# Performance work log

Measured on AMD Instinct MI355X. Metric: run time of the kernel, lower is better.

The kernel has to match this reference:

```python
import jax, jax.numpy as jnp
import numpy as np

NEG_SLOPE = 0.01  # jax.nn.leaky_relu default

def bicubic_resize(x, target_h, target_w):
    # NHWC bicubic resize with antialiasing (matches original module)
    b, h, w, c = x.shape
    return jax.image.resize(x, shape=(b, target_h, target_w, c), method='bicubic', antialias=True)

def setup_inputs() -> dict:
    key = jax.random.key(0)
    x = jax.random.normal(key, (16, 128, 128, 128), dtype=jnp.float32)  # NHWC
    return {"x": x, "in_size": 128, "out_size": 128}

def reference(x, in_size, out_size):
    y = bicubic_resize(x, 2 * in_size, 2 * in_size)
    # activation on the fine grid
    y = jax.nn.leaky_relu(y, negative_slope=NEG_SLOPE)
    # downsample (antialiased) back to out_size
    y = bicubic_resize(y, out_size, out_size)
    return y
```

## Files before the change

kernel.cpp:

```cpp
#include <hip/hip_runtime.h>


#define HH 128
#define WW 128
#define CC 128
#define RS 16
#define CH 16
#define PAD 132
#define NSTEP (RS + 4)

__device__ __forceinline__ double keys_cubic(double x) {
  if (x >= 2.0) return 0.0;
  if (x >= 1.0) return ((-0.5 * x + 2.5) * x - 4.0) * x + 2.0;
  return (1.5 * x - 2.5) * x * x + 1.0;
}

__global__ __launch_bounds__(256) void fused_updown_kernel(
    const float* __restrict__ x, float* __restrict__ out) {
  __shared__ __align__(16) float wUpV[256][4];
  __shared__ __align__(16) float wDnE[4][8];
  __shared__ __align__(16) float rowv[4][CH][PAD];

  const int tid = threadIdx.x;

  {
    const int k = tid;
    const double q = 0.5 * k - 0.25;
    const int st = ((k + 1) >> 1) - 2;
    double wr[4], s = 0.0;
#pragma unroll
    for (int i = 0; i < 4; ++i) {
      const int col = st + i;
      double w = (col >= 0 && col <= 127) ? keys_cubic(fabs((double)col - q)) : 0.0;
      wr[i] = w; s += w;
    }
    const double inv = 1.0 / s;
#pragma unroll
    for (int i = 0; i < 4; ++i) wUpV[k][i] = (float)(wr[i] * inv);
  }
  if (tid < 4) {
    const int e = tid;
    const int j = (e < 2) ? e : 124 + e;
    const double p = 2.0 * j + 0.5;
    const int st = 2 * j - 3;
    double wr[8], s = 0.0;
#pragma unroll
    for (int i = 0; i < 8; ++i) {
      const int col = st + i;
      double w = (col >= 0 && col <= 255) ? keys_cubic(0.5 * fabs((double)col - p)) : 0.0;
      wr[i] = w; s += w;
    }
    const double inv = 1.0 / s;
#pragma unroll
    for (int i = 0; i < 8; ++i) wDnE[e][i] = (float)(wr[i] * inv);
  }
  __syncthreads();

  const int bid = blockIdx.x;
  const int b = bid & 15;
  const int strip = (bid >> 4) & 7;
  const int chunk = bid >> 7;
  const int oy0 = strip * RS;
  const int c0 = chunk * CH;
  const int c = tid & 15;
  const int g = tid >> 4;
  const int col0 = g * 8;
  const bool gL = (g == 0), gR = (g == 15);

  const float* xbase = x + (size_t)b * (HH * WW * CC) + (size_t)col0 * CC + (c0 + c);
  float* obase = out + (size_t)b * (HH * WW * CC) + (size_t)col0 * CC + (c0 + c);
  const int m0 = oy0 - 2;

  auto load_row = [&](float (&d)[8], int row) {
    row = row < 0 ? 0 : (row > 127 ? 127 : row);
    const float* p = xbase + (size_t)row * (WW * CC);
#pragma unroll
    for (int j = 0; j < 8; ++j) d[j] = p[j * CC];
  };

  auto wdGet = [&](int oy, float cst, int tap) -> float {
    if (oy < 0 || oy > 127) return 0.f;
    if (oy < 2) return wDnE[oy][tap];
    if (oy > 125) return wDnE[oy - 124][tap];
    return cst;
  };

  auto proc = [&](int sl, const float (&vm)[8], float w0, float w1, float w2, float w3,
                  float (&B0)[8], float (&B1)[8], float (&B2)[8], float (&B3)[8]) {
    float v[16];
    if (!gL) {
      const float4 h = *(const float4*)&rowv[sl][c][col0 - 4];
      v[0] = h.x; v[1] = h.y; v[2] = h.z; v[3] = h.w;
    } else { v[0] = v[1] = v[2] = v[3] = 0.f; }
#pragma unroll
    for (int j = 0; j < 8; ++j) v[4 + j] = vm[j];
    if (!gR) {
      const float4 h = *(const float4*)&rowv[sl][c][col0 + 8];
      v[12] = h.x; v[13] = h.y; v[14] = h.z; v[15] = h.w;
    } else { v[12] = v[13] = v[14] = v[15] = 0.f; }

    float f[22];
#pragma unroll
    for (int u = 0; u < 22; ++u) {
      const int s = (u >> 1) + 1;
      float t;
      if (u & 1)
        t = fmaf(-0.0234375f, v[s], fmaf(0.2265625f, v[s + 1],
            fmaf(0.8671875f, v[s + 2], -0.0703125f * v[s + 3])));
      else
        t = fmaf(-0.0703125f, v[s], fmaf(0.8671875f, v[s + 1],
            fmaf(0.2265625f, v[s + 2], -0.0234375f * v[s + 3])));
      f[u] = fmaxf(t, 0.01f * t);
    }
    if (gL) {
#pragma unroll
      for (int u = 3; u <= 5; ++u) {
        const int s = (u >> 1) + 1;
        const float4 w = *(const float4*)wUpV[u - 3];
        const float t = fmaf(w.x, v[s], fmaf(w.y, v[s + 1],
                        fmaf(w.z, v[s + 2], w.w * v[s + 3])));
        f[u] = fmaxf(t, 0.01f * t);
      }
    }
    if (gR) {
#pragma unroll
      for (int u = 16; u <= 18; ++u) {
        const int s = (u >> 1) + 1;
        const float4 w = *(const float4*)wUpV[237 + u];
        const float t = fmaf(w.x, v[s], fmaf(w.y, v[s + 1],
                        fmaf(w.z, v[s + 2], w.w * v[s + 3])));
        f[u] = fmaxf(t, 0.01f * t);
      }
    }
    float tt[8];
#pragma unroll
    for (int jj = 0; jj < 8; ++jj) {
      tt[jj] = fmaf(-0.01171875f, f[2 * jj] + f[2 * jj + 7],
               fmaf(-0.03515625f, f[2 * jj + 1] + f[2 * jj + 6],
               fmaf(0.11328125f, f[2 * jj + 2] + f[2 * jj + 5],
                    0.43359375f * (f[2 * jj + 3] + f[2 * jj + 4]))));
    }
    if (gL) {
#pragma unroll
      for (int jj = 0; jj < 2; ++jj) {
        float s2 = 0.f;
#pragma unroll
        for (int i = 0; i < 8; ++i) s2 = fmaf(wDnE[jj][i], f[2 * jj + i], s2);
        tt[jj] = s2;
      }
    }
    if (gR) {
#pragma unroll
      for (int jj = 6; jj < 8; ++jj) {
        float s2 = 0.f;
#pragma unroll
        for (int i = 0; i < 8; ++i) s2 = fmaf(wDnE[jj - 4][i], f[2 * jj + i], s2);
        tt[jj] = s2;
      }
    }
#pragma unroll
    for (int jj = 0; jj < 8; ++jj) {
      B0[jj] = fmaf(w0, tt[jj], B0[jj]);
      B1[jj] = fmaf(w1, tt[jj], B1[jj]);
      B2[jj] = fmaf(w2, tt[jj], B2[jj]);
      B3[jj] = fmaf(w3, tt[jj], B3[jj]);
    }
  };

  float r0[8], r1[8], r2[8], r3[8], r4[8];
  float A0[8], A1[8], A2[8], A3[8], A4[8];
#pragma unroll
  for (int i = 0; i < 8; ++i) { A0[i]=0.f; A1[i]=0.f; A2[i]=0.f; A3[i]=0.f; A4[i]=0.f; }

  load_row(r0, m0 - 2);
  load_row(r1, m0 - 1);
  load_row(r2, m0);
  load_row(r3, m0 + 1);
  load_row(r4, m0 + 2);

  for (int t = 0; t < NSTEP; ++t) {
    const int m = m0 + t;
    if (t > 0) {
#pragma unroll
      for (int i = 0; i < 8; ++i) { r0[i]=r1[i]; r1[i]=r2[i]; r2[i]=r3[i]; r3[i]=r4[i]; }
      load_row(r4, m + 2);
    }
    const bool mOK = (m >= 0) && (m <= 127);
    const bool evOK = mOK && (t >= 1);
    const bool odOK = mOK && (t <= RS + 2);
    const int sp = (t & 1) * 2;
    float vE[8], vO[8];
    if (evOK) {
      const float4 wv = *(const float4*)wUpV[2 * m];
#pragma unroll
      for (int j = 0; j < 8; ++j)
        vE[j] = fmaf(wv.x, r0[j], fmaf(wv.y, r1[j], fmaf(wv.z, r2[j], wv.w * r3[j])));
      *(float4*)&rowv[sp][c][col0]     = make_float4(vE[0], vE[1], vE[2], vE[3]);
      *(float4*)&rowv[sp][c][col0 + 4] = make_float4(vE[4], vE[5], vE[6], vE[7]);
    }
    if (odOK) {
      const float4 wv = *(const float4*)wUpV[2 * m + 1];
#pragma unroll
      for (int j = 0; j < 8; ++j)
        vO[j] = fmaf(wv.x, r1[j], fmaf(wv.y, r2[j], fmaf(wv.z, r3[j], wv.w * r4[j])));
      *(float4*)&rowv[sp + 1][c][col0]     = make_float4(vO[0], vO[1], vO[2], vO[3]);
      *(float4*)&rowv[sp + 1][c][col0 + 4] = make_float4(vO[4], vO[5], vO[6], vO[7]);
    }
    __syncthreads();
    if (evOK)
      proc(sp, vE, wdGet(m - 2, -0.01171875f, 7), wdGet(m - 1, 0.11328125f, 5),
           wdGet(m, 0.43359375f, 3), wdGet(m + 1, -0.03515625f, 1),
           A0, A1, A2, A3);
    if (odOK)
      proc(sp + 1, vO, wdGet(m - 1, -0.03515625f, 6), wdGet(m, 0.43359375f, 4),
           wdGet(m + 1, 0.11328125f, 2), wdGet(m + 2, -0.01171875f, 0),
           A1, A2, A3, A4);
    if (m - 2 >= oy0) {
      float* op = obase + (size_t)(m - 2) * (WW * CC);
#pragma unroll
      for (int jj = 0; jj < 8; ++jj) op[jj * CC] = A0[jj];
    }
#pragma unroll
    for (int jj = 0; jj < 8; ++jj) { A0[jj]=A1[jj]; A1[jj]=A2[jj]; A2[jj]=A3[jj]; A3[jj]=A4[jj]; A4[jj]=0.f; }
  }
}

extern "C" void kernel_launch(void* const* d_in, const int* in_sizes, int n_in,
                              void* d_out, int out_size, void* d_ws, size_t ws_size,
                              hipStream_t stream) {
  const float* x = (const float*)d_in[0];
  float* o = (float*)d_out;
  dim3 grid(16 * 8 * 8);
  dim3 block(256);
  hipLaunchKernelGGL(fused_updown_kernel, grid, block, 0, stream, x, o);
}
```

Measured before the change: 105.1 us.

## Pack even/odd fine rows as float2 to use packed FP32 math

Computes the even and odd upsampled rows together and stores them as interleaved float2 in shared memory. The horizontal upsample, leaky ReLU and downsample then run on two-wide vectors, which the compiler can map to packed FP32 FMA instructions, and the halo reads and control flow are shared between the two rows. An extra input row is kept in registers, raising register pressure. A few boundary rows are now computed even when their result is discarded.

```diff
diff --git a/kernel.cpp b/kernel.cpp
--- a/kernel.cpp
+++ b/kernel.cpp
@@ -1,12 +1,14 @@
 #include <hip/hip_runtime.h>
 
+
+typedef float f2 __attribute__((ext_vector_type(2)));
 
 #define HH 128
 #define WW 128
 #define CC 128
 #define RS 16
 #define CH 16
-#define PAD 132
+#define PADF2 130
 #define NSTEP (RS + 4)
 
 __device__ __forceinline__ double keys_cubic(double x) {
@@ -19,7 +21,7 @@
     const float* __restrict__ x, float* __restrict__ out) {
   __shared__ __align__(16) float wUpV[256][4];
   __shared__ __align__(16) float wDnE[4][8];
-  __shared__ __align__(16) float rowv[4][CH][PAD];
+  __shared__ __align__(16) f2 rowv[2][CH][PADF2];
 
   const int tid = threadIdx.x;
 
@@ -85,89 +87,7 @@
     return cst;
   };
 
-  auto proc = [&](int sl, const float (&vm)[8], float w0, float w1, float w2, float w3,
-                  float (&B0)[8], float (&B1)[8], float (&B2)[8], float (&B3)[8]) {
-    float v[16];
-    if (!gL) {
-      const float4 h = *(const float4*)&rowv[sl][c][col0 - 4];
-      v[0] = h.x; v[1] = h.y; v[2] = h.z; v[3] = h.w;
-    } else { v[0] = v[1] = v[2] = v[3] = 0.f; }
-#pragma unroll
-    for (int j = 0; j < 8; ++j) v[4 + j] = vm[j];
-    if (!gR) {
-      const float4 h = *(const float4*)&rowv[sl][c][col0 + 8];
-      v[12] = h.x; v[13] = h.y; v[14] = h.z; v[15] = h.w;
-    } else { v[12] = v[13] = v[14] = v[15] = 0.f; }
-
-    float f[22];
-#pragma unroll
-    for (int u = 0; u < 22; ++u) {
-      const int s = (u >> 1) + 1;
-      float t;
-      if (u & 1)
-        t = fmaf(-0.0234375f, v[s], fmaf(0.2265625f, v[s + 1],
-            fmaf(0.8671875f, v[s + 2], -0.0703125f * v[s + 3])));
-      else
-        t = fmaf(-0.0703125f, v[s], fmaf(0.8671875f, v[s + 1],
-            fmaf(0.2265625f, v[s + 2], -0.0234375f * v[s + 3])));
-      f[u] = fmaxf(t, 0.01f * t);
-    }
-    if (gL) {
-#pragma unroll
-      for (int u = 3; u <= 5; ++u) {
-        const int s = (u >> 1) + 1;
-        const float4 w = *(const float4*)wUpV[u - 3];
-        const float t = fmaf(w.x, v[s], fmaf(w.y, v[s + 1],
-                        fmaf(w.z, v[s + 2], w.w * v[s + 3])));
-        f[u] = fmaxf(t, 0.01f * t);
-      }
-    }
-    if (gR) {
-#pragma unroll
-      for (int u = 16; u <= 18; ++u) {
-        const int s = (u >> 1) + 1;
-        const float4 w = *(const float4*)wUpV[237 + u];
-        const float t = fmaf(w.x, v[s], fmaf(w.y, v[s + 1],
-                        fmaf(w.z, v[s + 2], w.w * v[s + 3])));
-        f[u] = fmaxf(t, 0.01f * t);
-      }
-    }
-    float tt[8];
-#pragma unroll
-    for (int jj = 0; jj < 8; ++jj) {
-      tt[jj] = fmaf(-0.01171875f, f[2 * jj] + f[2 * jj + 7],
-               fmaf(-0.03515625f, f[2 * jj + 1] + f[2 * jj + 6],
-               fmaf(0.11328125f, f[2 * jj + 2] + f[2 * jj + 5],
-                    0.43359375f * (f[2 * jj + 3] + f[2 * jj + 4]))));
-    }
-    if (gL) {
-#pragma unroll
-      for (int jj = 0; jj < 2; ++jj) {
-        float s2 = 0.f;
-#pragma unroll
-        for (int i = 0; i < 8; ++i) s2 = fmaf(wDnE[jj][i], f[2 * jj + i], s2);
-        tt[jj] = s2;
-      }
-    }
-    if (gR) {
-#pragma unroll
-      for (int jj = 6; jj < 8; ++jj) {
-        float s2 = 0.f;
-#pragma unroll
-        for (int i = 0; i < 8; ++i) s2 = fmaf(wDnE[jj - 4][i], f[2 * jj + i], s2);
-        tt[jj] = s2;
-      }
-    }
-#pragma unroll
-    for (int jj = 0; jj < 8; ++jj) {
-      B0[jj] = fmaf(w0, tt[jj], B0[jj]);
-      B1[jj] = fmaf(w1, tt[jj], B1[jj]);
-      B2[jj] = fmaf(w2, tt[jj], B2[jj]);
-      B3[jj] = fmaf(w3, tt[jj], B3[jj]);
-    }
-  };
-
-  float r0[8], r1[8], r2[8], r3[8], r4[8];
+  float r0[8], r1[8], r2[8], r3[8], r4[8], r5[8];
   float A0[8], A1[8], A2[8], A3[8], A4[8];
 #pragma unroll
   for (int i = 0; i < 8; ++i) { A0[i]=0.f; A1[i]=0.f; A2[i]=0.f; A3[i]=0.f; A4[i]=0.f; }
@@ -177,51 +97,137 @@
   load_row(r2, m0);
   load_row(r3, m0 + 1);
   load_row(r4, m0 + 2);
+  load_row(r5, m0 + 3);
 
   for (int t = 0; t < NSTEP; ++t) {
     const int m = m0 + t;
     if (t > 0) {
 #pragma unroll
-      for (int i = 0; i < 8; ++i) { r0[i]=r1[i]; r1[i]=r2[i]; r2[i]=r3[i]; r3[i]=r4[i]; }
-      load_row(r4, m + 2);
+      for (int i = 0; i < 8; ++i) {
+        r0[i]=r1[i]; r1[i]=r2[i]; r2[i]=r3[i]; r3[i]=r4[i]; r4[i]=r5[i];
+      }
+      load_row(r5, m + 3);
     }
     const bool mOK = (m >= 0) && (m <= 127);
-    const bool evOK = mOK && (t >= 1);
-    const bool odOK = mOK && (t <= RS + 2);
-    const int sp = (t & 1) * 2;
-    float vE[8], vO[8];
-    if (evOK) {
-      const float4 wv = *(const float4*)wUpV[2 * m];
-#pragma unroll
-      for (int j = 0; j < 8; ++j)
-        vE[j] = fmaf(wv.x, r0[j], fmaf(wv.y, r1[j], fmaf(wv.z, r2[j], wv.w * r3[j])));
-      *(float4*)&rowv[sp][c][col0]     = make_float4(vE[0], vE[1], vE[2], vE[3]);
-      *(float4*)&rowv[sp][c][col0 + 4] = make_float4(vE[4], vE[5], vE[6], vE[7]);
-    }
-    if (odOK) {
-      const float4 wv = *(const float4*)wUpV[2 * m + 1];
-#pragma unroll
-      for (int j = 0; j < 8; ++j)
-        vO[j] = fmaf(wv.x, r1[j], fmaf(wv.y, r2[j], fmaf(wv.z, r3[j], wv.w * r4[j])));
-      *(float4*)&rowv[sp + 1][c][col0]     = make_float4(vO[0], vO[1], vO[2], vO[3]);
-      *(float4*)&rowv[sp + 1][c][col0 + 4] = make_float4(vO[4], vO[5], vO[6], vO[7]);
+    const int sp = t & 1;
+    f2 vown[8];
+    if (mOK) {
+      const float4 we = *(const float4*)wUpV[2 * m];
+      const float4 wo = *(const float4*)wUpV[2 * m + 1];
+#pragma unroll
+      for (int j = 0; j < 8; ++j) {
+        vown[j].x = fmaf(we.x, r0[j], fmaf(we.y, r1[j], fmaf(we.z, r2[j], we.w * r3[j])));
+        vown[j].y = fmaf(wo.x, r1[j], fmaf(wo.y, r2[j], fmaf(wo.z, r3[j], wo.w * r4[j])));
+      }
+#pragma unroll
+      for (int j = 0; j < 8; ++j) rowv[sp][c][col0 + j] = vown[j];
     }
     __syncthreads();
-    if (evOK)
-      proc(sp, vE, wdGet(m - 2, -0.01171875f, 7), wdGet(m - 1, 0.11328125f, 5),
-           wdGet(m, 0.43359375f, 3), wdGet(m + 1, -0.03515625f, 1),
-           A0, A1, A2, A3);
-    if (odOK)
-      proc(sp + 1, vO, wdGet(m - 1, -0.03515625f, 6), wdGet(m, 0.43359375f, 4),
-           wdGet(m + 1, 0.11328125f, 2), wdGet(m + 2, -0.01171875f, 0),
-           A1, A2, A3, A4);
+    if (mOK) {
+      f2 vv[16];
+      if (!gL) {
+#pragma unroll
+        for (int i = 0; i < 4; ++i) vv[i] = rowv[sp][c][col0 - 4 + i];
+      } else {
+#pragma unroll
+        for (int i = 0; i < 4; ++i) vv[i] = f2{0.f, 0.f};
+      }
+#pragma unroll
+      for (int j = 0; j < 8; ++j) vv[4 + j] = vown[j];
+      if (!gR) {
+#pragma unroll
+        for (int i = 0; i < 4; ++i) vv[12 + i] = rowv[sp][c][col0 + 8 + i];
+      } else {
+#pragma unroll
+        for (int i = 0; i < 4; ++i) vv[12 + i] = f2{0.f, 0.f};
+      }
+
+      f2 ff[22];
+#pragma unroll
+      for (int u = 0; u < 22; ++u) {
+        const int s = (u >> 1) + 1;
+        f2 t2;
+        if (u & 1)
+          t2 = vv[s] * (-0.0234375f) + vv[s + 1] * 0.2265625f
+             + vv[s + 2] * 0.8671875f + vv[s + 3] * (-0.0703125f);
+        else
+          t2 = vv[s] * (-0.0703125f) + vv[s + 1] * 0.8671875f
+             + vv[s + 2] * 0.2265625f + vv[s + 3] * (-0.0234375f);
+        ff[u] = __builtin_elementwise_max(t2, t2 * 0.01f);
+      }
+      if (gL) {
+#pragma unroll
+        for (int u = 3; u <= 5; ++u) {
+          const int s = (u >> 1) + 1;
+          const float4 w = *(const float4*)wUpV[u - 3];
+          f2 t2 = vv[s] * w.x + vv[s + 1] * w.y + vv[s + 2] * w.z + vv[s + 3] * w.w;
+          ff[u] = __builtin_elementwise_max(t2, t2 * 0.01f);
+        }
+      }
+      if (gR) {
+#pragma unroll
+        for (int u = 16; u <= 18; ++u) {
+          const int s = (u >> 1) + 1;
+          const float4 w = *(const float4*)wUpV[237 + u];
+          f2 t2 = vv[s] * w.x + vv[s + 1] * w.y + vv[s + 2] * w.z + vv[s + 3] * w.w;
+          ff[u] = __builtin_elementwise_max(t2, t2 * 0.01f);
+        }
+      }
+
+      f2 tt[8];
+#pragma unroll
+      for (int jj = 0; jj < 8; ++jj) {
+        tt[jj] = (ff[2*jj]     + ff[2*jj + 7]) * (-0.01171875f)
+               + (ff[2*jj + 1] + ff[2*jj + 6]) * (-0.03515625f)
+               + (ff[2*jj + 2] + ff[2*jj + 5]) * 0.11328125f
+               + (ff[2*jj + 3] + ff[2*jj + 4]) * 0.43359375f;
+      }
+      if (gL) {
+#pragma unroll
+        for (int jj = 0; jj < 2; ++jj) {
+          f2 s2 = f2{0.f, 0.f};
+#pragma unroll
+          for (int i = 0; i < 8; ++i) s2 += ff[2*jj + i] * wDnE[jj][i];
+          tt[jj] = s2;
+        }
+      }
+      if (gR) {
+#pragma unroll
+        for (int jj = 6; jj < 8; ++jj) {
+          f2 s2 = f2{0.f, 0.f};
+#pragma unroll
+          for (int i = 0; i < 8; ++i) s2 += ff[2*jj + i] * wDnE[jj - 4][i];
+          tt[jj] = s2;
+        }
+      }
+
+      const float wE0 = wdGet(m - 2, -0.01171875f, 7);
+      const float wE1 = wdGet(m - 1, 0.11328125f, 5);
+      const float wE2 = wdGet(m, 0.43359375f, 3);
+      const float wE3 = wdGet(m + 1, -0.03515625f, 1);
+      const float wO0 = wdGet(m - 1, -0.03515625f, 6);
+      const float wO1 = wdGet(m, 0.43359375f, 4);
+      const float wO2 = wdGet(m + 1, 0.11328125f, 2);
+      const float wO3 = wdGet(m + 2, -0.01171875f, 0);
+#pragma unroll
+      for (int jj = 0; jj < 8; ++jj) {
+        const float te = tt[jj].x, to = tt[jj].y;
+        A0[jj] = fmaf(wE0, te, A0[jj]);
+        A1[jj] = fmaf(wE1, te, fmaf(wO0, to, A1[jj]));
+        A2[jj] = fmaf(wE2, te, fmaf(wO1, to, A2[jj]));
+        A3[jj] = fmaf(wE3, te, fmaf(wO2, to, A3[jj]));
+        A4[jj] = fmaf(wO3, to, A4[jj]);
+      }
+    }
     if (m - 2 >= oy0) {
       float* op = obase + (size_t)(m - 2) * (WW * CC);
 #pragma unroll
       for (int jj = 0; jj < 8; ++jj) op[jj * CC] = A0[jj];
     }
 #pragma unroll
-    for (int jj = 0; jj < 8; ++jj) { A0[jj]=A1[jj]; A1[jj]=A2[jj]; A2[jj]=A3[jj]; A3[jj]=A4[jj]; A4[jj]=0.f; }
+    for (int jj = 0; jj < 8; ++jj) {
+      A0[jj]=A1[jj]; A1[jj]=A2[jj]; A2[jj]=A3[jj]; A3[jj]=A4[jj]; A4[jj]=0.f;
+    }
   }
 }
 
```

Result: no change. 106.2 us (+1.1%).
